# Performance work log

Hardware: AMD Instinct MI355X
Metric: run time of the kernel (lower is better)

The kernel has to match this reference:

```python
import jax, jax.numpy as jnp
import numpy as np

CHUNK_SIZE = 64
EPS = 1e-6


def setup_inputs() -> dict:
    key = jax.random.key(0)
    ks = jax.random.split(key, 5)
    B, NH, S, DH = 2, 16, 4096, 64
    return {
        "q": jax.random.normal(ks[0], (B, NH, S, DH), dtype=jnp.float32),
        "k": jax.random.normal(ks[1], (B, NH, S, DH), dtype=jnp.float32),
        "v": jax.random.normal(ks[2], (B, NH, S, DH), dtype=jnp.float32),
        "igate_preact": jax.random.normal(ks[3], (B, NH, S), dtype=jnp.float32),
        "fgate_preact": jax.random.normal(ks[4], (B, NH, S), dtype=jnp.float32),
    }


def _mlstm_intra(q, k, v, ig, fg, chunk_size, eps):
    # q,k,v: [B,NH,S,DH]; ig,fg: [B,NH,S]
    B, NH, S, DH = q.shape
    L = chunk_size
    NC = S // L
    qc = q.reshape(B, NH, NC, L, DH)
    kc = k.reshape(B, NH, NC, L, DH)
    vc = v.reshape(B, NH, NC, L, DH)
    igc = ig.reshape(B, NH, NC, L)
    fgc = fg.reshape(B, NH, NC, L)

    # log forget gates and their within-chunk cumulative sums
    log_fg = jax.nn.log_sigmoid(fgc)                      # [B,NH,NC,L]
    log_fg_cum = jnp.cumsum(log_fg, axis=-1)              # [B,NH,NC,L]

    # gated decay matrix: logD[i,j] = sum_{t=j+1..i} log f_t + i_j  for j<=i
    log_fg_mat = log_fg_cum[..., :, None] - log_fg_cum[..., None, :]  # [B,NH,NC,L,L]
    log_D = log_fg_mat + igc[..., None, :]
    causal = jnp.tril(jnp.ones((L, L), dtype=bool))
    log_D = jnp.where(causal, log_D, -jnp.inf)

    # stabilizer (row-wise max)
    m = jnp.max(log_D, axis=-1)                           # [B,NH,NC,L]
    D = jnp.exp(log_D - m[..., None])                     # [B,NH,NC,L,L]

    # QK scores scaled, gated by decay matrix
    scale = 1.0 / jnp.sqrt(jnp.asarray(DH, dtype=q.dtype))
    scores = jnp.einsum("bncld,bncsd->bncls", qc, kc) * scale
    C = scores * D                                        # [B,NH,NC,L,L]

    # stabilized normalizer: max(|row sum|, exp(-m))
    n = jnp.maximum(jnp.abs(jnp.sum(C, axis=-1)), jnp.exp(-m))  # [B,NH,NC,L]
    h = jnp.einsum("bncls,bncsd->bncld", C, vc) / (n[..., None] + eps)
    return h.reshape(B, NH, S, DH)


def reference(q, k, v, igate_preact, fgate_preact):
    return _mlstm_intra(q, k, v, igate_preact, fgate_preact, CHUNK_SIZE, EPS)
```

## Files before the change

### kernel.cpp

```cpp
#include <hip/hip_runtime.h>
#include <hip/hip_bf16.h>
#include <math.h>

namespace {

typedef __bf16 bf16x8 __attribute__((ext_vector_type(8)));
typedef float f32x4 __attribute__((ext_vector_type(4)));

constexpr int L = 64;
constexpr int DH = 64;

__device__ __forceinline__ int swz(int row, int col) {
  return row * 128 + ((((col >> 3) ^ (row & 7)) << 4)) + (col & 7) * 2;
}

__device__ __forceinline__ unsigned short bfbits(float f) {
  __bf16 h = (__bf16)f;
  return __builtin_bit_cast(unsigned short, h);
}
__device__ __forceinline__ __bf16 tobf(float f) { return (__bf16)f; }

__global__ __launch_bounds__(64) void mlstm_mfma(
    const float* __restrict__ q, const float* __restrict__ k,
    const float* __restrict__ v, const float* __restrict__ ig,
    const float* __restrict__ fg, float* __restrict__ out) {

  __shared__ __align__(16) char vt_raw[64 * 128];
  __shared__ __align__(16) char cs_raw[64 * 128];
  __shared__ float ea_sh[64], eb_sh[64], em_sh[64], inv_sh[64];

  const int lane = threadIdx.x;
  const int m = lane & 15;
  const int g = lane >> 4;
  const size_t cbase = (size_t)blockIdx.x * (L * DH);

  {
    const size_t gb = (size_t)blockIdx.x * L;
    const float x = fg[gb + lane];
    const float lf = fminf(x, 0.f) - log1pf(__expf(-fabsf(x)));
    float cum = lf;
#pragma unroll
    for (int o = 1; o < 64; o <<= 1) {
      const float t = __shfl_up(cum, o, 64);
      if (lane >= o) cum += t;
    }
    const float a = ig[gb + lane] - cum;
    float b = a;
#pragma unroll
    for (int o = 1; o < 64; o <<= 1) {
      const float t = __shfl_up(b, o, 64);
      if (lane >= o) b = fmaxf(b, t);
    }
    const float bmax = __shfl(b, 63, 64);
    ea_sh[lane] = 0.125f * __expf(a - bmax);
    eb_sh[lane] = __expf(bmax - b);
    em_sh[lane] = __expf(-(b + cum));
  }

  {
    const float4* v4 = (const float4*)(v + cbase);
    float4 buf[16];
#pragma unroll
    for (int it = 0; it < 16; ++it) buf[it] = v4[it * 64 + lane];
    unsigned short* vt = (unsigned short*)vt_raw;
#pragma unroll
    for (int it = 0; it < 16; ++it) {
      const int idx = it * 64 + lane;
      const int j = idx >> 4;
      const int d0 = (idx & 15) * 4;
      vt[swz(d0 + 0, j) >> 1] = bfbits(buf[it].x);
      vt[swz(d0 + 1, j) >> 1] = bfbits(buf[it].y);
      vt[swz(d0 + 2, j) >> 1] = bfbits(buf[it].z);
      vt[swz(d0 + 3, j) >> 1] = bfbits(buf[it].w);
    }
  }

  bf16x8 kf[4][2], qf[4][2];
#pragma unroll
  for (int rb = 0; rb < 4; ++rb)
#pragma unroll
    for (int kb = 0; kb < 2; ++kb) {
      const int off = (rb * 16 + m) * 64 + kb * 32 + g * 8;
      const float4 k0 = *(const float4*)(k + cbase + off);
      const float4 k1 = *(const float4*)(k + cbase + off + 4);
      const float4 q0 = *(const float4*)(q + cbase + off);
      const float4 q1 = *(const float4*)(q + cbase + off + 4);
      kf[rb][kb] = bf16x8{tobf(k0.x), tobf(k0.y), tobf(k0.z), tobf(k0.w),
                          tobf(k1.x), tobf(k1.y), tobf(k1.z), tobf(k1.w)};
      qf[rb][kb] = bf16x8{tobf(q0.x), tobf(q0.y), tobf(q0.z), tobf(q0.w),
                          tobf(q1.x), tobf(q1.y), tobf(q1.z), tobf(q1.w)};
    }

  f32x4 st[4][4];
#pragma unroll
  for (int cb = 0; cb < 4; ++cb)
#pragma unroll
    for (int rb = 0; rb < 4; ++rb) {
      if (rb > cb) continue;
      f32x4 acc = {0.f, 0.f, 0.f, 0.f};
      acc = __builtin_amdgcn_mfma_f32_16x16x32_bf16(kf[rb][0], qf[cb][0], acc, 0, 0, 0);
      acc = __builtin_amdgcn_mfma_f32_16x16x32_bf16(kf[rb][1], qf[cb][1], acc, 0, 0, 0);
      st[rb][cb] = acc;
    }

  float ea_j[4][4];
#pragma unroll
  for (int rb = 0; rb < 4; ++rb)
#pragma unroll
    for (int e = 0; e < 4; ++e) ea_j[rb][e] = ea_sh[rb * 16 + g * 4 + e];

#pragma unroll
  for (int cb = 0; cb < 4; ++cb) {
    const int i = cb * 16 + m;
    const float ebv = eb_sh[i];
    float rs = 0.f;
#pragma unroll
    for (int rb = 0; rb < 4; ++rb) {
      unsigned long long wp = 0ull;
      if (rb <= cb) {
#pragma unroll
        for (int e = 0; e < 4; ++e) {
          const int j = rb * 16 + g * 4 + e;
          const float val =
              (j <= i) ? st[rb][cb][e] * ea_j[rb][e] * ebv : 0.f;
          rs += val;
          wp |= (unsigned long long)bfbits(val) << (16 * e);
        }
      }
      *(unsigned long long*)(cs_raw + swz(i, rb * 16 + g * 4)) = wp;
    }
    rs += __shfl_xor(rs, 16, 64);
    rs += __shfl_xor(rs, 32, 64);
    const float n = fmaxf(fabsf(rs), em_sh[i]);
    inv_sh[i] = 1.f / (n + 1e-6f);
  }

  bf16x8 vfr[4][2];
#pragma unroll
  for (int db = 0; db < 4; ++db)
#pragma unroll
    for (int jb = 0; jb < 2; ++jb)
      vfr[db][jb] =
          *(const bf16x8*)(vt_raw + swz(db * 16 + m, jb * 32 + g * 8));

  bf16x8 cfr[4][2];
#pragma unroll
  for (int ib = 0; ib < 4; ++ib) {
    cfr[ib][0] = *(const bf16x8*)(cs_raw + swz(ib * 16 + m, g * 8));
    if (ib >= 2)
      cfr[ib][1] = *(const bf16x8*)(cs_raw + swz(ib * 16 + m, 32 + g * 8));
  }

  f32x4 hh[4][4];
#pragma unroll
  for (int ib = 0; ib < 4; ++ib)
#pragma unroll
    for (int db = 0; db < 4; ++db) {
      f32x4 acc = {0.f, 0.f, 0.f, 0.f};
      acc = __builtin_amdgcn_mfma_f32_16x16x32_bf16(vfr[db][0], cfr[ib][0], acc, 0, 0, 0);
      if (ib >= 2)
        acc = __builtin_amdgcn_mfma_f32_16x16x32_bf16(vfr[db][1], cfr[ib][1], acc, 0, 0, 0);
      hh[ib][db] = acc;
    }

#pragma unroll
  for (int ib = 0; ib < 4; ++ib) {
    const int i = ib * 16 + m;
    const float iv = inv_sh[i];
    float* op = out + cbase + i * 64 + g * 4;
#pragma unroll
    for (int db = 0; db < 4; ++db) {
      const f32x4 hv = hh[ib][db];
      *(float4*)(op + db * 16) =
          make_float4(hv[0] * iv, hv[1] * iv, hv[2] * iv, hv[3] * iv);
    }
  }
}

}

extern "C" void kernel_launch(void* const* d_in, const int* in_sizes, int n_in,
                              void* d_out, int out_size, void* d_ws,
                              size_t ws_size, hipStream_t stream) {
  const float* q = (const float*)d_in[0];
  const float* k = (const float*)d_in[1];
  const float* v = (const float*)d_in[2];
  const float* ig = (const float*)d_in[3];
  const float* fg = (const float*)d_in[4];
  float* out = (float*)d_out;

  const int total = in_sizes[0];
  const int nchunks = total / (L * DH);
  mlstm_mfma<<<dim3(nchunks), dim3(64), 0, stream>>>(q, k, v, ig, fg, out);
}
```

Baseline: 27.63 us.

## Share one LDS tile for V and C, reorder loads, keep normalizer in registers

Issues all global loads (gates, V, Q, K) up front before the gate scan so memory latency overlaps the shuffle-based scan. V is transposed into a single LDS tile, read back into registers, and the same tile is then reused for the C matrix, halving shared memory. The per-row normalizer stays in registers instead of going through LDS, and the second MFMA stage is computed and stored per row block to shrink live accumulators. Reusing the tile relies on the wave's own ordering, since this is a single-wave block, and holding the V fragments longer may raise register pressure.

```diff
diff --git a/kernel.cpp b/kernel.cpp
--- a/kernel.cpp
+++ b/kernel.cpp
@@ -11,7 +11,7 @@
 constexpr int DH = 64;
 
 __device__ __forceinline__ int swz(int row, int col) {
-  return row * 128 + ((((col >> 3) ^ (row & 7)) << 4)) + (col & 7) * 2;
+  return row * 128 + (((col >> 3) ^ (row & 7)) << 4) + (col & 7) * 2;
 }
 
 __device__ __forceinline__ unsigned short bfbits(float f) {
@@ -25,55 +25,22 @@
     const float* __restrict__ v, const float* __restrict__ ig,
     const float* __restrict__ fg, float* __restrict__ out) {
 
-  __shared__ __align__(16) char vt_raw[64 * 128];
-  __shared__ __align__(16) char cs_raw[64 * 128];
-  __shared__ float ea_sh[64], eb_sh[64], em_sh[64], inv_sh[64];
+  __shared__ __align__(16) char tile[64 * 128];
+  __shared__ float ea_sh[64], eb_sh[64], em_sh[64];
 
   const int lane = threadIdx.x;
   const int m = lane & 15;
   const int g = lane >> 4;
   const size_t cbase = (size_t)blockIdx.x * (L * DH);
+  const size_t gb = (size_t)blockIdx.x * L;
 
-  {
-    const size_t gb = (size_t)blockIdx.x * L;
-    const float x = fg[gb + lane];
-    const float lf = fminf(x, 0.f) - log1pf(__expf(-fabsf(x)));
-    float cum = lf;
+  const float fgv = fg[gb + lane];
+  const float igv = ig[gb + lane];
+
+  const float4* v4 = (const float4*)(v + cbase);
+  float4 vbuf[16];
 #pragma unroll
-    for (int o = 1; o < 64; o <<= 1) {
-      const float t = __shfl_up(cum, o, 64);
-      if (lane >= o) cum += t;
-    }
-    const float a = ig[gb + lane] - cum;
-    float b = a;
-#pragma unroll
-    for (int o = 1; o < 64; o <<= 1) {
-      const float t = __shfl_up(b, o, 64);
-      if (lane >= o) b = fmaxf(b, t);
-    }
-    const float bmax = __shfl(b, 63, 64);
-    ea_sh[lane] = 0.125f * __expf(a - bmax);
-    eb_sh[lane] = __expf(bmax - b);
-    em_sh[lane] = __expf(-(b + cum));
-  }
-
-  {
-    const float4* v4 = (const float4*)(v + cbase);
-    float4 buf[16];
-#pragma unroll
-    for (int it = 0; it < 16; ++it) buf[it] = v4[it * 64 + lane];
-    unsigned short* vt = (unsigned short*)vt_raw;
-#pragma unroll
-    for (int it = 0; it < 16; ++it) {
-      const int idx = it * 64 + lane;
-      const int j = idx >> 4;
-      const int d0 = (idx & 15) * 4;
-      vt[swz(d0 + 0, j) >> 1] = bfbits(buf[it].x);
-      vt[swz(d0 + 1, j) >> 1] = bfbits(buf[it].y);
-      vt[swz(d0 + 2, j) >> 1] = bfbits(buf[it].z);
-      vt[swz(d0 + 3, j) >> 1] = bfbits(buf[it].w);
-    }
-  }
+  for (int it = 0; it < 16; ++it) vbuf[it] = v4[it * 64 + lane];
 
   bf16x8 kf[4][2], qf[4][2];
 #pragma unroll
@@ -90,6 +57,48 @@
       qf[rb][kb] = bf16x8{tobf(q0.x), tobf(q0.y), tobf(q0.z), tobf(q0.w),
                           tobf(q1.x), tobf(q1.y), tobf(q1.z), tobf(q1.w)};
     }
+
+  {
+    const float lf = fminf(fgv, 0.f) - log1pf(__expf(-fabsf(fgv)));
+    float cum = lf;
+#pragma unroll
+    for (int o = 1; o < 64; o <<= 1) {
+      const float t = __shfl_up(cum, o, 64);
+      if (lane >= o) cum += t;
+    }
+    const float a = igv - cum;
+    float b = a;
+#pragma unroll
+    for (int o = 1; o < 64; o <<= 1) {
+      const float t = __shfl_up(b, o, 64);
+      if (lane >= o) b = fmaxf(b, t);
+    }
+    const float bmax = __shfl(b, 63, 64);
+    ea_sh[lane] = 0.125f * __expf(a - bmax);
+    eb_sh[lane] = __expf(bmax - b);
+    em_sh[lane] = __expf(-(b + cum));
+  }
+
+  {
+    unsigned short* vt = (unsigned short*)tile;
+#pragma unroll
+    for (int it = 0; it < 16; ++it) {
+      const int idx = it * 64 + lane;
+      const int j = idx >> 4;
+      const int d0 = (idx & 15) * 4;
+      vt[swz(d0 + 0, j) >> 1] = bfbits(vbuf[it].x);
+      vt[swz(d0 + 1, j) >> 1] = bfbits(vbuf[it].y);
+      vt[swz(d0 + 2, j) >> 1] = bfbits(vbuf[it].z);
+      vt[swz(d0 + 3, j) >> 1] = bfbits(vbuf[it].w);
+    }
+  }
+
+  bf16x8 vfr[4][2];
+#pragma unroll
+  for (int db = 0; db < 4; ++db)
+#pragma unroll
+    for (int jb = 0; jb < 2; ++jb)
+      vfr[db][jb] = *(const bf16x8*)(tile + swz(db * 16 + m, jb * 32 + g * 8));
 
   f32x4 st[4][4];
 #pragma unroll
@@ -109,6 +118,7 @@
 #pragma unroll
     for (int e = 0; e < 4; ++e) ea_j[rb][e] = ea_sh[rb * 16 + g * 4 + e];
 
+  float invr[4];
 #pragma unroll
   for (int cb = 0; cb < 4; ++cb) {
     const int i = cb * 16 + m;
@@ -121,56 +131,40 @@
 #pragma unroll
         for (int e = 0; e < 4; ++e) {
           const int j = rb * 16 + g * 4 + e;
-          const float val =
-              (j <= i) ? st[rb][cb][e] * ea_j[rb][e] * ebv : 0.f;
+          const float val = (j <= i) ? st[rb][cb][e] * ea_j[rb][e] * ebv : 0.f;
           rs += val;
           wp |= (unsigned long long)bfbits(val) << (16 * e);
         }
       }
-      *(unsigned long long*)(cs_raw + swz(i, rb * 16 + g * 4)) = wp;
+      *(unsigned long long*)(tile + swz(i, rb * 16 + g * 4)) = wp;
     }
     rs += __shfl_xor(rs, 16, 64);
     rs += __shfl_xor(rs, 32, 64);
     const float n = fmaxf(fabsf(rs), em_sh[i]);
-    inv_sh[i] = 1.f / (n + 1e-6f);
+    invr[cb] = 1.f / (n + 1e-6f);
   }
-
-  bf16x8 vfr[4][2];
-#pragma unroll
-  for (int db = 0; db < 4; ++db)
-#pragma unroll
-    for (int jb = 0; jb < 2; ++jb)
-      vfr[db][jb] =
-          *(const bf16x8*)(vt_raw + swz(db * 16 + m, jb * 32 + g * 8));
-
-  bf16x8 cfr[4][2];
-#pragma unroll
-  for (int ib = 0; ib < 4; ++ib) {
-    cfr[ib][0] = *(const bf16x8*)(cs_raw + swz(ib * 16 + m, g * 8));
-    if (ib >= 2)
-      cfr[ib][1] = *(const bf16x8*)(cs_raw + swz(ib * 16 + m, 32 + g * 8));
-  }
-
-  f32x4 hh[4][4];
-#pragma unroll
-  for (int ib = 0; ib < 4; ++ib)
-#pragma unroll
-    for (int db = 0; db < 4; ++db) {
-      f32x4 acc = {0.f, 0.f, 0.f, 0.f};
-      acc = __builtin_amdgcn_mfma_f32_16x16x32_bf16(vfr[db][0], cfr[ib][0], acc, 0, 0, 0);
-      if (ib >= 2)
-        acc = __builtin_amdgcn_mfma_f32_16x16x32_bf16(vfr[db][1], cfr[ib][1], acc, 0, 0, 0);
-      hh[ib][db] = acc;
-    }
 
 #pragma unroll
   for (int ib = 0; ib < 4; ++ib) {
     const int i = ib * 16 + m;
-    const float iv = inv_sh[i];
+    const bf16x8 c0 = *(const bf16x8*)(tile + swz(i, g * 8));
+    f32x4 acc[4];
+#pragma unroll
+    for (int db = 0; db < 4; ++db) {
+      f32x4 z = {0.f, 0.f, 0.f, 0.f};
+      acc[db] = __builtin_amdgcn_mfma_f32_16x16x32_bf16(vfr[db][0], c0, z, 0, 0, 0);
+    }
+    if (ib >= 2) {
+      const bf16x8 c1 = *(const bf16x8*)(tile + swz(i, 32 + g * 8));
+#pragma unroll
+      for (int db = 0; db < 4; ++db)
+        acc[db] = __builtin_amdgcn_mfma_f32_16x16x32_bf16(vfr[db][1], c1, acc[db], 0, 0, 0);
+    }
+    const float iv = invr[ib];
     float* op = out + cbase + i * 64 + g * 4;
 #pragma unroll
     for (int db = 0; db < 4; ++db) {
-      const f32x4 hv = hh[ib][db];
+      const f32x4 hv = acc[db];
       *(float4*)(op + db * 16) =
           make_float4(hv[0] * iv, hv[1] * iv, hv[2] * iv, hv[3] * iv);
     }
```

Measured after the change: 28.21 us. 1.02x slower.
